# Performance work log

Hardware: AMD Instinct MI355X
Metric: run time of the kernel (lower is better)

Reference implementation:

```python
import jax, jax.numpy as jnp
import numpy as np

N = 10000       # nodes (atoms)
E = 160000      # edges (avg degree 16)
NE = 10         # num_elements
C = 64          # hidden scalar channels (hidden_irreps 0e multiplicity)
NB = 8          # num_bessel
SH = 9          # spherical-harmonic dim for max_ell=2 (1+3+5)
MLPH = 16       # readout MLP hidden (MLP_irreps)
T = 2           # num_interactions
R_MAX = 5.0
P_CUT = 6       # num_polynomial_cutoff
AVG_NEIGH = 32.0


def _sph(u):
    # real spherical harmonics up to l=2, e3nn 'component' normalization
    x, y, z = u[:, 0], u[:, 1], u[:, 2]
    s3, s5, s15 = 3.0 ** 0.5, 5.0 ** 0.5, 15.0 ** 0.5
    return jnp.stack([
        jnp.ones_like(x),
        s3 * x, s3 * y, s3 * z,
        s15 * x * y, s15 * y * z, (s5 / 2) * (3 * z * z - 1),
        s15 * x * z, (s15 / 2) * (x * x - y * y)], axis=-1)


def _radial(r):
    # Bessel radial basis * smooth polynomial cutoff (RadialEmbeddingBlock)
    n = jnp.arange(1, NB + 1, dtype=r.dtype)
    bessel = (2.0 / R_MAX) ** 0.5 * jnp.sin(n * jnp.pi * r[:, None] / R_MAX) / r[:, None]
    x = jnp.clip(r / R_MAX, 0.0, 1.0)
    p = P_CUT
    fc = (1.0 - 0.5 * (p + 1) * (p + 2) * x ** p
          + p * (p + 2) * x ** (p + 1)
          - 0.5 * p * (p + 1) * x ** (p + 2))
    fc = jnp.where(x < 1.0, fc, 0.0)
    return bessel * fc[:, None]


def setup_inputs():
    key = jax.random.key(0)
    ks = jax.random.split(key, 14)
    positions = jax.random.normal(ks[0], (N, 3), jnp.float32) * 3.0
    node_attrs = jax.nn.one_hot(jax.random.randint(ks[1], (N,), 0, NE), NE, dtype=jnp.float32)
    edge_index = jax.random.randint(ks[2], (2, E), 0, N)
    shifts = jnp.zeros((E, 3), jnp.float32)

    def g(k, shape, fan):
        return jax.random.normal(k, shape, jnp.float32) / np.sqrt(fan)

    params = dict(
        atomic_energies=jax.random.normal(ks[3], (NE,), jnp.float32),
        W_embed=g(ks[4], (NE, C), NE),          # LinearNodeEmbeddingBlock
        W_up=g(ks[5], (T, C, C), C),            # linear_up per interaction
        W_r1=g(ks[6], (T, NB, MLPH), NB),       # radial MLP layer 1
        W_r2=g(ks[7], (T, MLPH, C * SH), MLPH), # radial MLP -> TP weights
        W_mix=g(ks[8], (T, C, SH, C), C * SH),  # post-scatter linear mixing
        W_self=g(ks[9], (T, C, C), C),          # self/skip connection
        w_read=g(ks[10], (C,), C),              # LinearReadoutBlock
        W_mlp1=g(ks[11], (C, MLPH), C),         # NonLinearReadoutBlock
        w_mlp2=g(ks[12], (MLPH,), MLPH),
    )
    return dict(positions=positions, node_attrs=node_attrs, shifts=shifts,
                edge_index=edge_index, **params)


def reference(positions, node_attrs, shifts, atomic_energies, W_embed, W_up,
              W_r1, W_r2, W_mix, W_self, w_read, W_mlp1, w_mlp2, edge_index):
    snd, rcv = edge_index[0], edge_index[1]
    vec = positions[rcv] - positions[snd] + shifts              # [E,3]
    r = jnp.linalg.norm(vec, axis=-1) + 1e-9                    # [E]
    sh = _sph(vec / r[:, None])                                 # [E,SH]
    edge_feats = _radial(r)                                     # [E,NB]

    h = node_attrs @ W_embed                                    # [N,C] node embedding
    reps = [node_attrs @ atomic_energies]                       # node_e0
    for t in range(T):
        h_up = h @ W_up[t]                                      # [N,C]
        # radial-MLP produced tensor-product weights, one per (channel, sh) path
        tp_w = (jax.nn.silu(edge_feats @ W_r1[t]) @ W_r2[t]).reshape(-1, C, SH)
        # gather -> edge-wise tensor product -> scatter-reduce (the hot loop)
        msg = tp_w * h_up[snd][:, :, None] * sh[:, None, :]     # [E,C,SH]
        agg = jax.ops.segment_sum(msg, rcv, num_segments=N) / AVG_NEIGH
        h = jnp.einsum('ncs,cso->no', agg, W_mix[t]) + h @ W_self[t]
        if t < T - 1:
            reps.append(h @ w_read)                             # linear readout
        else:
            reps.append(jax.nn.silu(h @ W_mlp1) @ w_mlp2)       # nonlinear readout
    return jnp.stack(reps, axis=0)  # [T+1, N] per-layer atomic energy contributions
```

## Files before the change

### kernel.cpp

```cpp
#include <hip/hip_runtime.h>
#include <math.h>

#define N_NODES 10000
#define N_EDGES 160000
#define NEL 10
#define C 64
#define NB 8
#define SHD 9
#define MLPH 16
#define CSH 576
#define R_MAX 5.0f
#define INV_AVG 0.03125f
#define SCAN_CH 40
#define WBASE (N_EDGES - 2 * 8 * CSH)
#define WB2   (WBASE - 10240)
#define WB3   (WB2 - 1024)
#define ROWP  584

typedef _Float16 f16x2 __attribute__((ext_vector_type(2)));
typedef _Float16 f16x8 __attribute__((ext_vector_type(8)));
typedef float    f32x4 __attribute__((ext_vector_type(4)));
typedef _Float16 half_t;

__device__ __forceinline__ float silu_f(float v) {
    return v / (1.0f + __expf(-v));
}

__device__ __forceinline__ float dot2f(f16x2 a, f16x2 b, float c) {
#if __has_builtin(__builtin_amdgcn_fdot2)
    return __builtin_amdgcn_fdot2(a, b, c, false);
#else
    return c + (float)a.x * (float)b.x + (float)a.y * (float)b.y;
#endif
}

__global__ __launch_bounds__(256) void k_zero(
    int* __restrict__ cnt, int* __restrict__ deg)
{
    int i = blockIdx.x * 256 + threadIdx.x;
    if (i == 0) *cnt = 0;
    if (i < N_NODES) deg[i] = 0;
}

__global__ __launch_bounds__(256) void k_edge(
    const float* __restrict__ pos, const float* __restrict__ shifts,
    const int* __restrict__ ei,
    const float* __restrict__ na, const float* __restrict__ We,
    const float* __restrict__ ae,
    int* __restrict__ cnt, int* __restrict__ deg,
    int* __restrict__ act_snd, int* __restrict__ act_rcv,
    float* __restrict__ act_u, float* __restrict__ act_ef,
    half_t* __restrict__ hh, float* __restrict__ out)
{
    int i = blockIdx.x * 256 + threadIdx.x;
    int lane = threadIdx.x & 63;

    {
        int n = i >> 6;
        float acc = 0.0f, e0 = 0.0f;
        #pragma unroll
        for (int k = 0; k < NEL; k++) {
            float a = na[n * NEL + k];
            acc += a * We[k * C + lane];
            e0 += a * ae[k];
        }
        hh[i] = (half_t)acc;
        if (lane == 0) out[n] = e0;
    }

    if (blockIdx.x >= N_EDGES / 256) return;
    int e = i;
    int snd = ei[e];
    int rcv = ei[N_EDGES + e];
    float vx = pos[rcv * 3 + 0] - pos[snd * 3 + 0] + shifts[e * 3 + 0];
    float vy = pos[rcv * 3 + 1] - pos[snd * 3 + 1] + shifts[e * 3 + 1];
    float vz = pos[rcv * 3 + 2] - pos[snd * 3 + 2] + shifts[e * 3 + 2];
    float r = sqrtf(vx * vx + vy * vy + vz * vz) + 1e-9f;
    float x = r / R_MAX;
    bool active = x < 1.0f;

    unsigned long long m = __ballot(active);
    int base = 0;
    if (m) {
        int leader = __ffsll((unsigned long long)m) - 1;
        if (lane == leader) base = atomicAdd(cnt, __popcll(m));
        base = __shfl(base, leader);
    }
    if (!active) return;

    int p = base + __popcll(m & ((1ull << lane) - 1ull));
    act_snd[p] = snd;
    act_rcv[p] = rcv;
    atomicAdd(&deg[rcv], 1);

    float inv_r = 1.0f / r;
    *(float4*)&act_u[p * 4] = make_float4(vx * inv_r, vy * inv_r, vz * inv_r, r);

    float x6 = x * x * x; x6 = x6 * x6;
    float x7 = x6 * x;
    float x8 = x7 * x;
    float fc = 1.0f - 28.0f * x6 + 48.0f * x7 - 21.0f * x8;
    float theta = 3.14159265358979323846f * r / R_MAX;
    float s1 = sinf(theta), c1 = cosf(theta);
    float sn = s1, cn = c1;
    float scale = 0.6324555320336759f * inv_r * fc;
    float ef[NB];
    ef[0] = scale * sn;
    #pragma unroll
    for (int n = 1; n < NB; n++) {
        float sn1 = sn * c1 + cn * s1;
        float cn1 = cn * c1 - sn * s1;
        sn = sn1; cn = cn1;
        ef[n] = scale * sn;
    }
    *(float4*)&act_ef[p * 8 + 0] = make_float4(ef[0], ef[1], ef[2], ef[3]);
    *(float4*)&act_ef[p * 8 + 4] = make_float4(ef[4], ef[5], ef[6], ef[7]);
}

__global__ __launch_bounds__(256) void k_scan(
    const int* __restrict__ deg, int* __restrict__ rowptr, int* __restrict__ cursor)
{
    __shared__ int dl[N_NODES];
    __shared__ int part[256];
    int tid = threadIdx.x;
    for (int i = tid; i < N_NODES; i += 256) dl[i] = deg[i];
    __syncthreads();

    int base = tid * SCAN_CH;
    int s = 0;
    #pragma unroll 8
    for (int i = 0; i < SCAN_CH; i++) {
        int idx = base + i;
        if (idx < N_NODES) s += dl[idx];
    }
    part[tid] = s;
    __syncthreads();
    for (int off = 1; off < 256; off <<= 1) {
        int v = (tid >= off) ? part[tid - off] : 0;
        __syncthreads();
        part[tid] += v;
        __syncthreads();
    }
    int run = part[tid] - s;
    for (int i = 0; i < SCAN_CH; i++) {
        int idx = base + i;
        if (idx < N_NODES) {
            int v = dl[idx];
            dl[idx] = run;
            run += v;
        }
    }
    __syncthreads();
    for (int i = tid; i < N_NODES; i += 256) {
        int r = dl[i];
        rowptr[i] = r;
        cursor[i] = r;
    }
    if (tid == 255) rowptr[N_NODES] = part[255];
}

__global__ __launch_bounds__(256) void k_rank(
    const int* __restrict__ cnt, const int* __restrict__ act_rcv,
    const float* __restrict__ Wr2, const float* __restrict__ Wmix,
    const float* __restrict__ Wself, const float* __restrict__ Wup,
    int* __restrict__ cursor, f16x2* __restrict__ wlth,
    f16x8* __restrict__ wmixf, f16x8* __restrict__ wupf, int* __restrict__ perm)
{
    int i = blockIdx.x * 256 + threadIdx.x;
    int nAct = *cnt;

    if (i >= WBASE) {
        int idx = i - WBASE;
        int t = idx / (8 * CSH);
        int r = idx - t * (8 * CSH);
        int mq = r / CSH, j = r - mq * CSH;
        int c = j & 63, s = j >> 6;
        float lo = Wr2[t * MLPH * CSH + (2 * mq + 0) * CSH + c * SHD + s];
        float hi = Wr2[t * MLPH * CSH + (2 * mq + 1) * CSH + c * SHD + s];
        f16x2 v; v.x = (_Float16)lo; v.y = (_Float16)hi;
        wlth[idx] = v;
    } else if (i >= WB2) {
        int idx = i - WB2;
        int t = idx / 5120;
        int r = idx - t * 5120;
        int ks = r >> 8;
        int rr = r & 255;
        int nt = rr >> 6;
        int ln = rr & 63;
        f16x8 v;
        #pragma unroll
        for (int e = 0; e < 8; e++) {
            int k = ks * 32 + ((ln >> 4) << 3) + e;
            int col = nt * 16 + (ln & 15);
            float x;
            if (k < CSH)
                x = Wmix[(size_t)t * CSH * C + ((k & 63) * SHD + (k >> 6)) * C + col] * INV_AVG;
            else
                x = Wself[(size_t)t * C * C + (k - CSH) * C + col];
            v[e] = (_Float16)x;
        }
        wmixf[(size_t)((t * 20 + ks) * 4 + nt) * 64 + ln] = v;
    } else if (i >= WB3) {
        int idx = i - WB3;
        int t = idx >> 9;
        int r = idx & 511;
        int ks = r >> 8;
        int rr = r & 255;
        int nt = rr >> 6;
        int ln = rr & 63;
        f16x8 v;
        #pragma unroll
        for (int e = 0; e < 8; e++) {
            int k = ks * 32 + ((ln >> 4) << 3) + e;
            int col = nt * 16 + (ln & 15);
            v[e] = (_Float16)Wup[(size_t)t * C * C + k * C + col];
        }
        wupf[(size_t)((t * 2 + ks) * 4 + nt) * 64 + ln] = v;
    }
    if (i >= nAct) return;
    int pos = atomicAdd(&cursor[act_rcv[i]], 1);
    perm[pos] = i;
}

__global__ __launch_bounds__(256) void k_permute(
    const int* __restrict__ cnt, const int* __restrict__ perm,
    const int* __restrict__ act_snd, const int* __restrict__ act_rcv,
    const float* __restrict__ act_u, const float* __restrict__ act_ef,
    const float* __restrict__ Wr1,
    int* __restrict__ csnd, int* __restrict__ crcv, float* __restrict__ csh,
    f16x2* __restrict__ chidh0, f16x2* __restrict__ chidh1)
{
    int p = blockIdx.x * 256 + threadIdx.x;
    if (p >= *cnt) return;
    int i = perm[p];

    csnd[p] = act_snd[i];
    crcv[p] = act_rcv[i];

    float4 u4 = *(const float4*)&act_u[i * 4];
    float ux = u4.x, uy = u4.y, uz = u4.z;
    const float s3 = 1.7320508075688772f;
    const float s5 = 2.23606797749979f;
    const float s15 = 3.872983346207417f;
    *(float4*)&csh[p * 16 + 0] = make_float4(1.0f, s3 * ux, s3 * uy, s3 * uz);
    *(float4*)&csh[p * 16 + 4] = make_float4(s15 * ux * uy, s15 * uy * uz,
                                             0.5f * s5 * (3.0f * uz * uz - 1.0f),
                                             s15 * ux * uz);
    csh[p * 16 + 8] = 0.5f * s15 * (ux * ux - uy * uy);

    float4 e0 = *(const float4*)&act_ef[i * 8 + 0];
    float4 e1 = *(const float4*)&act_ef[i * 8 + 4];
    float ef[NB] = {e0.x, e0.y, e0.z, e0.w, e1.x, e1.y, e1.z, e1.w};

    #pragma unroll
    for (int t = 0; t < 2; t++) {
        f16x2* dst = (t == 0) ? chidh0 : chidh1;
        const float* W = Wr1 + t * NB * MLPH;
        f16x2 hv2[8];
        #pragma unroll
        for (int mp = 0; mp < 8; mp++) {
            float a0 = 0.0f, a1 = 0.0f;
            #pragma unroll
            for (int b = 0; b < NB; b++) {
                float efb = ef[b];
                a0 += efb * W[b * MLPH + 2 * mp + 0];
                a1 += efb * W[b * MLPH + 2 * mp + 1];
            }
            f16x2 v; v.x = (_Float16)silu_f(a0); v.y = (_Float16)silu_f(a1);
            hv2[mp] = v;
        }
        *(float4*)&dst[p * 8 + 0] = *(float4*)&hv2[0];
        *(float4*)&dst[p * 8 + 4] = *(float4*)&hv2[4];
    }
}

__global__ __launch_bounds__(64) void k_upm(
    const half_t* __restrict__ hh, const f16x8* __restrict__ wupf,
    float* __restrict__ hup)
{
    int lane = threadIdx.x & 63;
    int base = blockIdx.x * 16;
    int rowA = base + (lane & 15);
    int kg = (lane >> 4) << 3;

    f32x4 u0 = {0.f,0.f,0.f,0.f}, u1 = {0.f,0.f,0.f,0.f};
    f32x4 u2 = {0.f,0.f,0.f,0.f}, u3 = {0.f,0.f,0.f,0.f};
    const half_t* hrow = hh + (size_t)rowA * C + kg;
    #pragma unroll
    for (int ks = 0; ks < 2; ks++) {
        f16x8 a = *(const f16x8*)(hrow + ks * 32);
        const f16x8* bp = wupf + (size_t)(ks * 4) * 64 + lane;
        u0 = __builtin_amdgcn_mfma_f32_16x16x32_f16(a, bp[0],   u0, 0, 0, 0);
        u1 = __builtin_amdgcn_mfma_f32_16x16x32_f16(a, bp[64],  u1, 0, 0, 0);
        u2 = __builtin_amdgcn_mfma_f32_16x16x32_f16(a, bp[128], u2, 0, 0, 0);
        u3 = __builtin_amdgcn_mfma_f32_16x16x32_f16(a, bp[192], u3, 0, 0, 0);
    }
    int colb = lane & 15;
    int rowb = base + ((lane >> 4) << 2);
    #pragma unroll
    for (int r = 0; r < 4; r++) {
        float* hp = hup + (size_t)(rowb + r) * C + colb;
        hp[0]  = u0[r];
        hp[16] = u1[r];
        hp[32] = u2[r];
        hp[48] = u3[r];
    }
}

template <int RMODE>
__global__ __launch_bounds__(256) void k_fuse(
    const int* __restrict__ rowptr, const int* __restrict__ csnd,
    const int* __restrict__ crcv, const float* __restrict__ csh,
    const f16x2* __restrict__ chh, const f16x2* __restrict__ wlth,
    const float* __restrict__ hup_in, const f16x8* __restrict__ wf,
    const f16x8* __restrict__ wupf1, half_t* __restrict__ hh,
    const float* __restrict__ wread, const float* __restrict__ Wm1,
    const float* __restrict__ wm2,
    float* __restrict__ hup_out, float* __restrict__ rep)
{
    __shared__ half_t Hs[16 * ROWP];
    __shared__ half_t Hs2[16 * 72];

    int lane = threadIdx.x & 63;
    int w = threadIdx.x >> 6;
    int bbase = blockIdx.x * 16;
    int n0 = bbase + w * 4;
    int beg = rowptr[n0], end = rowptr[n0 + 4];

    f16x2 wreg[8][9];
    #pragma unroll
    for (int mq = 0; mq < 8; mq++)
        #pragma unroll
        for (int jj = 0; jj < 9; jj++)
            wreg[mq][jj] = wlth[mq * CSH + (jj << 6) + lane];

    float acc[9];
    int curRcv = -1;

#define FLUSH() { half_t* ag = &Hs[(curRcv - bbase) * ROWP + lane]; \
    _Pragma("unroll") for (int jj = 0; jj < 9; jj++) ag[jj << 6] = (half_t)acc[jj]; }
#define ZFILL(FROM, TO) for (int zn = (FROM); zn < (TO); zn++) { \
    half_t* ag = &Hs[(zn - bbase) * ROWP + lane]; \
    _Pragma("unroll") for (int jj = 0; jj < 9; jj++) ag[jj << 6] = (half_t)0.0f; }

    for (int k0 = beg; k0 < end; k0 += 4) {
        int nv = end - k0; if (nv > 4) nv = 4;

#define PRE(Q) int kc##Q = (k0 + Q < end) ? k0 + Q : end - 1; \
        int rcvq##Q = crcv[kc##Q]; \
        float hupq##Q = hup_in[csnd[kc##Q] * C + lane];
        PRE(0) PRE(1) PRE(2) PRE(3)
#undef PRE

        float tw0[9], tw1[9], tw2[9], tw3[9];
        #pragma unroll
        for (int jj = 0; jj < 9; jj++) {
            tw0[jj] = 0.f; tw1[jj] = 0.f; tw2[jj] = 0.f; tw3[jj] = 0.f;
        }

        #pragma unroll
        for (int mq = 0; mq < 8; mq++) {
            f16x2 h0 = chh[kc0 * 8 + mq], h1 = chh[kc1 * 8 + mq];
            f16x2 h2 = chh[kc2 * 8 + mq], h3 = chh[kc3 * 8 + mq];
            #pragma unroll
            for (int jj = 0; jj < 9; jj++) {
                f16x2 wv = wreg[mq][jj];
                tw0[jj] = dot2f(h0, wv, tw0[jj]);
                tw1[jj] = dot2f(h1, wv, tw1[jj]);
                tw2[jj] = dot2f(h2, wv, tw2[jj]);
                tw3[jj] = dot2f(h3, wv, tw3[jj]);
            }
        }

#define SCAT(Q) if (Q < nv) { \
        int rcv = rcvq##Q; \
        float hupS = hupq##Q; \
        float4 sA = *(const float4*)&csh[kc##Q * 16]; \
        float4 sB = *(const float4*)&csh[kc##Q * 16 + 4]; \
        float s8v = csh[kc##Q * 16 + 8]; \
        float sh9[9] = {sA.x, sA.y, sA.z, sA.w, sB.x, sB.y, sB.z, sB.w, s8v}; \
        if (rcv != curRcv) { \
            if (curRcv >= 0) { FLUSH(); ZFILL(curRcv + 1, rcv) } else { ZFILL(n0, rcv) } \
            curRcv = rcv; \
            _Pragma("unroll") for (int jj = 0; jj < 9; jj++) acc[jj] = tw##Q[jj] * (hupS * sh9[jj]); \
        } else { \
            _Pragma("unroll") for (int jj = 0; jj < 9; jj++) acc[jj] += tw##Q[jj] * (hupS * sh9[jj]); \
        } }
        SCAT(0) SCAT(1) SCAT(2) SCAT(3)
#undef SCAT
    }

    int zfrom = n0;
    if (curRcv >= 0) { FLUSH(); zfrom = curRcv + 1; }
    ZFILL(zfrom, n0 + 4)
#undef FLUSH
#undef ZFILL

    __syncthreads();

    int rowL = lane & 15;
    int kg = (lane >> 4) << 3;
    f32x4 acc4 = {0.f, 0.f, 0.f, 0.f};
    const half_t* hrow = hh + (size_t)(bbase + rowL) * C + kg;
    #pragma unroll
    for (int ks = 0; ks < 20; ks++) {
        f16x8 a = (ks < 18) ? *(const f16x8*)&Hs[rowL * ROWP + ks * 32 + kg]
                            : *(const f16x8*)(hrow + (ks - 18) * 32);
        f16x8 b = wf[(size_t)(ks * 4 + w) * 64 + lane];
        acc4 = __builtin_amdgcn_mfma_f32_16x16x32_f16(a, b, acc4, 0, 0, 0);
    }

    int colb = lane & 15;
    int rq = (lane >> 4) << 2;

    __syncthreads();

    if (RMODE == 0) {
        #pragma unroll
        for (int r = 0; r < 4; r++)
            Hs2[(rq + r) * 72 + w * 16 + colb] = (half_t)acc4[r];
        __syncthreads();

        if (w == 0) {
            int row = lane & 15, seg = lane >> 4;
            float v = 0.0f;
            #pragma unroll
            for (int j = 0; j < 16; j++)
                v += (float)Hs2[row * 72 + seg * 16 + j] * wread[seg * 16 + j];
            v += __shfl_xor(v, 16);
            v += __shfl_xor(v, 32);
            if (seg == 0) rep[bbase + row] = v;
        }

        {
            int idx = threadIdx.x;
            if (idx < 128) {
                int row = idx >> 3, cq = idx & 7;
                *(float4*)&hh[(size_t)(bbase + row) * C + cq * 8] =
                    *(const float4*)&Hs2[row * 72 + cq * 8];
            }
        }

        f32x4 u = {0.f, 0.f, 0.f, 0.f};
        #pragma unroll
        for (int ks = 0; ks < 2; ks++) {
            f16x8 a = *(const f16x8*)&Hs2[rowL * 72 + ks * 32 + kg];
            f16x8 b = wupf1[(size_t)(ks * 4 + w) * 64 + lane];
            u = __builtin_amdgcn_mfma_f32_16x16x32_f16(a, b, u, 0, 0, 0);
        }
        #pragma unroll
        for (int r = 0; r < 4; r++)
            hup_out[(size_t)(bbase + rq + r) * C + w * 16 + colb] = u[r];
    } else {
        float* Hn = (float*)Hs;
        float* W1l = (float*)Hs + 16 * 68;
        for (int t = threadIdx.x; t < C * MLPH; t += 256) W1l[t] = Wm1[t];
        #pragma unroll
        for (int r = 0; r < 4; r++)
            Hn[(rq + r) * 68 + w * 16 + colb] = acc4[r];
        __syncthreads();

        int n = threadIdx.x >> 4, m = threadIdx.x & 15;
        float a2 = 0.0f;
        #pragma unroll 8
        for (int c = 0; c < C; c++) a2 += Hn[n * 68 + c] * W1l[c * MLPH + m];
        float rv = silu_f(a2) * wm2[m];
        rv += __shfl_xor(rv, 1); rv += __shfl_xor(rv, 2);
        rv += __shfl_xor(rv, 4); rv += __shfl_xor(rv, 8);
        if (m == 0) rep[bbase + n] = rv;
    }
}

extern "C" void kernel_launch(void* const* d_in, const int* in_sizes, int n_in,
                              void* d_out, int out_size, void* d_ws, size_t ws_size,
                              hipStream_t stream) {
    const float* pos    = (const float*)d_in[0];
    const float* na     = (const float*)d_in[1];
    const float* shifts = (const float*)d_in[2];
    const int*   ei     = (const int*)d_in[3];
    const float* ae     = (const float*)d_in[4];
    const float* We     = (const float*)d_in[5];
    const float* Wup    = (const float*)d_in[6];
    const float* Wr1    = (const float*)d_in[7];
    const float* Wr2    = (const float*)d_in[8];
    const float* Wmix   = (const float*)d_in[9];
    const float* Wself  = (const float*)d_in[10];
    const float* wread  = (const float*)d_in[11];
    const float* Wm1    = (const float*)d_in[12];
    const float* wm2    = (const float*)d_in[13];
    float* out = (float*)d_out;

    char* ws = (char*)d_ws;
    size_t off = 0;
    auto alloc = [&](size_t bytes) {
        off = (off + 255) & ~(size_t)255;
        void* p = ws + off;
        off += bytes;
        return p;
    };
    int*   cnt     = (int*)alloc(4);
    int*   deg     = (int*)alloc((size_t)N_NODES * 4);
    int*   rowptr  = (int*)alloc((size_t)(N_NODES + 1) * 4);
    int*   cursor  = (int*)alloc((size_t)N_NODES * 4);
    f16x2* wlth    = (f16x2*)alloc((size_t)2 * 8 * CSH * 4);
    f16x8* wmixf   = (f16x8*)alloc((size_t)2 * 5120 * 16);
    f16x8* wupf    = (f16x8*)alloc((size_t)1024 * 16);
    int*   perm    = (int*)alloc((size_t)N_EDGES * 4);
    int*   act_snd = (int*)alloc((size_t)N_EDGES * 4);
    int*   act_rcv = (int*)alloc((size_t)N_EDGES * 4);
    float* act_u   = (float*)alloc((size_t)N_EDGES * 4 * 4);
    float* act_ef  = (float*)alloc((size_t)N_EDGES * 8 * 4);
    int*   csnd    = (int*)alloc((size_t)N_EDGES * 4);
    int*   crcv    = (int*)alloc((size_t)N_EDGES * 4);
    float* csh     = (float*)alloc((size_t)N_EDGES * 16 * 4);
    f16x2* chidh0  = (f16x2*)alloc((size_t)N_EDGES * 8 * 4);
    f16x2* chidh1  = (f16x2*)alloc((size_t)N_EDGES * 8 * 4);
    float* hup     = (float*)alloc((size_t)N_NODES * C * 4);
    float* hup2    = (float*)alloc((size_t)N_NODES * C * 4);
    half_t* hh     = (half_t*)alloc((size_t)N_NODES * C * 2);

    k_zero<<<(N_NODES + 255) / 256, 256, 0, stream>>>(cnt, deg);

    k_edge<<<(N_NODES * C) / 256, 256, 0, stream>>>(pos, shifts, ei, na, We, ae,
                                                    cnt, deg, act_snd, act_rcv,
                                                    act_u, act_ef, hh, out);
    k_scan<<<1, 256, 0, stream>>>(deg, rowptr, cursor);
    k_rank<<<N_EDGES / 256, 256, 0, stream>>>(cnt, act_rcv, Wr2, Wmix, Wself, Wup,
                                              cursor, wlth, wmixf, wupf, perm);
    k_permute<<<N_EDGES / 256, 256, 0, stream>>>(cnt, perm, act_snd, act_rcv,
                                                 act_u, act_ef, Wr1,
                                                 csnd, crcv, csh, chidh0, chidh1);
    k_upm<<<N_NODES / 16, 64, 0, stream>>>(hh, wupf, hup);

    k_fuse<0><<<N_NODES / 16, 256, 0, stream>>>(rowptr, csnd, crcv, csh,
                                                chidh0, wlth, hup,
                                                wmixf, wupf + 512, hh,
                                                wread, Wm1, wm2,
                                                hup2, out + N_NODES);

    k_fuse<1><<<N_NODES / 16, 256, 0, stream>>>(rowptr, csnd, crcv, csh,
                                                chidh1, wlth + 8 * CSH, hup2,
                                                wmixf + 5120, wupf + 512, hh,
                                                wread, Wm1, wm2,
                                                hup, out + 2 * N_NODES);
}
```

Before: 123.4 us.

## Merge rank and permute into one atomic scatter, halve nodes per fuse block

Weight repacking moves into the spare blocks of k_edge. The separate k_rank and k_permute kernels are replaced by a single k_scatter that claims its CSR slot with an atomicAdd and writes the permuted edge data directly, removing the perm array and one launch. k_fuse now handles 8 nodes per block instead of 16, doubling the grid to improve load balance and occupancy. The cost is that the 16-row MFMA tiles are half wasted, and edge order within a node's segment is now nondeterministic.

```diff
diff --git a/kernel.cpp b/kernel.cpp
--- a/kernel.cpp
+++ b/kernel.cpp
@@ -12,10 +12,8 @@
 #define R_MAX 5.0f
 #define INV_AVG 0.03125f
 #define SCAN_CH 40
-#define WBASE (N_EDGES - 2 * 8 * CSH)
-#define WB2   (WBASE - 10240)
-#define WB3   (WB2 - 1024)
 #define ROWP  584
+#define NPB   8
 
 typedef _Float16 f16x2 __attribute__((ext_vector_type(2)));
 typedef _Float16 f16x8 __attribute__((ext_vector_type(8)));
@@ -47,9 +45,12 @@
     const int* __restrict__ ei,
     const float* __restrict__ na, const float* __restrict__ We,
     const float* __restrict__ ae,
+    const float* __restrict__ Wr2, const float* __restrict__ Wmix,
+    const float* __restrict__ Wself, const float* __restrict__ Wup,
     int* __restrict__ cnt, int* __restrict__ deg,
     int* __restrict__ act_snd, int* __restrict__ act_rcv,
     float* __restrict__ act_u, float* __restrict__ act_ef,
+    f16x2* __restrict__ wlth, f16x8* __restrict__ wmixf, f16x8* __restrict__ wupf,
     half_t* __restrict__ hh, float* __restrict__ out)
 {
     int i = blockIdx.x * 256 + threadIdx.x;
@@ -68,7 +69,58 @@
         if (lane == 0) out[n] = e0;
     }
 
-    if (blockIdx.x >= N_EDGES / 256) return;
+    if (blockIdx.x >= N_EDGES / 256) {
+        int idx = i - N_EDGES;
+        if (idx < 2 * 8 * CSH) {
+            int t = idx / (8 * CSH);
+            int r = idx - t * (8 * CSH);
+            int mq = r / CSH, j = r - mq * CSH;
+            int c = j & 63, s = j >> 6;
+            float lo = Wr2[t * MLPH * CSH + (2 * mq + 0) * CSH + c * SHD + s];
+            float hi = Wr2[t * MLPH * CSH + (2 * mq + 1) * CSH + c * SHD + s];
+            f16x2 v; v.x = (_Float16)lo; v.y = (_Float16)hi;
+            wlth[idx] = v;
+        } else if (idx < 2 * 8 * CSH + 10240) {
+            int k2 = idx - 2 * 8 * CSH;
+            int t = k2 / 5120;
+            int r = k2 - t * 5120;
+            int ks = r >> 8;
+            int rr = r & 255;
+            int nt = rr >> 6;
+            int ln = rr & 63;
+            f16x8 v;
+            #pragma unroll
+            for (int e = 0; e < 8; e++) {
+                int k = ks * 32 + ((ln >> 4) << 3) + e;
+                int col = nt * 16 + (ln & 15);
+                float x;
+                if (k < CSH)
+                    x = Wmix[(size_t)t * CSH * C + ((k & 63) * SHD + (k >> 6)) * C + col] * INV_AVG;
+                else
+                    x = Wself[(size_t)t * C * C + (k - CSH) * C + col];
+                v[e] = (_Float16)x;
+            }
+            wmixf[(size_t)((t * 20 + ks) * 4 + nt) * 64 + ln] = v;
+        } else if (idx < 2 * 8 * CSH + 10240 + 1024) {
+            int k2 = idx - (2 * 8 * CSH + 10240);
+            int t = k2 >> 9;
+            int r = k2 & 511;
+            int ks = r >> 8;
+            int rr = r & 255;
+            int nt = rr >> 6;
+            int ln = rr & 63;
+            f16x8 v;
+            #pragma unroll
+            for (int e = 0; e < 8; e++) {
+                int k = ks * 32 + ((ln >> 4) << 3) + e;
+                int col = nt * 16 + (ln & 15);
+                v[e] = (_Float16)Wup[(size_t)t * C * C + k * C + col];
+            }
+            wupf[(size_t)((t * 2 + ks) * 4 + nt) * 64 + ln] = v;
+        }
+        return;
+    }
+
     int e = i;
     int snd = ei[e];
     int rcv = ei[N_EDGES + e];
@@ -159,83 +211,21 @@
     if (tid == 255) rowptr[N_NODES] = part[255];
 }
 
-__global__ __launch_bounds__(256) void k_rank(
-    const int* __restrict__ cnt, const int* __restrict__ act_rcv,
-    const float* __restrict__ Wr2, const float* __restrict__ Wmix,
-    const float* __restrict__ Wself, const float* __restrict__ Wup,
-    int* __restrict__ cursor, f16x2* __restrict__ wlth,
-    f16x8* __restrict__ wmixf, f16x8* __restrict__ wupf, int* __restrict__ perm)
-{
-    int i = blockIdx.x * 256 + threadIdx.x;
-    int nAct = *cnt;
-
-    if (i >= WBASE) {
-        int idx = i - WBASE;
-        int t = idx / (8 * CSH);
-        int r = idx - t * (8 * CSH);
-        int mq = r / CSH, j = r - mq * CSH;
-        int c = j & 63, s = j >> 6;
-        float lo = Wr2[t * MLPH * CSH + (2 * mq + 0) * CSH + c * SHD + s];
-        float hi = Wr2[t * MLPH * CSH + (2 * mq + 1) * CSH + c * SHD + s];
-        f16x2 v; v.x = (_Float16)lo; v.y = (_Float16)hi;
-        wlth[idx] = v;
-    } else if (i >= WB2) {
-        int idx = i - WB2;
-        int t = idx / 5120;
-        int r = idx - t * 5120;
-        int ks = r >> 8;
-        int rr = r & 255;
-        int nt = rr >> 6;
-        int ln = rr & 63;
-        f16x8 v;
-        #pragma unroll
-        for (int e = 0; e < 8; e++) {
-            int k = ks * 32 + ((ln >> 4) << 3) + e;
-            int col = nt * 16 + (ln & 15);
-            float x;
-            if (k < CSH)
-                x = Wmix[(size_t)t * CSH * C + ((k & 63) * SHD + (k >> 6)) * C + col] * INV_AVG;
-            else
-                x = Wself[(size_t)t * C * C + (k - CSH) * C + col];
-            v[e] = (_Float16)x;
-        }
-        wmixf[(size_t)((t * 20 + ks) * 4 + nt) * 64 + ln] = v;
-    } else if (i >= WB3) {
-        int idx = i - WB3;
-        int t = idx >> 9;
-        int r = idx & 511;
-        int ks = r >> 8;
-        int rr = r & 255;
-        int nt = rr >> 6;
-        int ln = rr & 63;
-        f16x8 v;
-        #pragma unroll
-        for (int e = 0; e < 8; e++) {
-            int k = ks * 32 + ((ln >> 4) << 3) + e;
-            int col = nt * 16 + (ln & 15);
-            v[e] = (_Float16)Wup[(size_t)t * C * C + k * C + col];
-        }
-        wupf[(size_t)((t * 2 + ks) * 4 + nt) * 64 + ln] = v;
-    }
-    if (i >= nAct) return;
-    int pos = atomicAdd(&cursor[act_rcv[i]], 1);
-    perm[pos] = i;
-}
-
-__global__ __launch_bounds__(256) void k_permute(
-    const int* __restrict__ cnt, const int* __restrict__ perm,
-    const int* __restrict__ act_snd, const int* __restrict__ act_rcv,
-    const float* __restrict__ act_u, const float* __restrict__ act_ef,
-    const float* __restrict__ Wr1,
+__global__ __launch_bounds__(256) void k_scatter(
+    const int* __restrict__ cnt, const int* __restrict__ act_snd,
+    const int* __restrict__ act_rcv, const float* __restrict__ act_u,
+    const float* __restrict__ act_ef, const float* __restrict__ Wr1,
+    int* __restrict__ cursor,
     int* __restrict__ csnd, int* __restrict__ crcv, float* __restrict__ csh,
     f16x2* __restrict__ chidh0, f16x2* __restrict__ chidh1)
 {
-    int p = blockIdx.x * 256 + threadIdx.x;
-    if (p >= *cnt) return;
-    int i = perm[p];
+    int i = blockIdx.x * 256 + threadIdx.x;
+    if (i >= *cnt) return;
+    int rcv = act_rcv[i];
+    int p = atomicAdd(&cursor[rcv], 1);
 
     csnd[p] = act_snd[i];
-    crcv[p] = act_rcv[i];
+    crcv[p] = rcv;
 
     float4 u4 = *(const float4*)&act_u[i * 4];
     float ux = u4.x, uy = u4.y, uz = u4.z;
@@ -318,14 +308,16 @@
     const float* __restrict__ wm2,
     float* __restrict__ hup_out, float* __restrict__ rep)
 {
-    __shared__ half_t Hs[16 * ROWP];
-    __shared__ half_t Hs2[16 * 72];
+    __shared__ half_t Hs[NPB * ROWP];
+    __shared__ half_t Hs2[NPB * 72];
+    __shared__ float  Hn[NPB * 68];
+    __shared__ float  W1l[C * MLPH];
 
     int lane = threadIdx.x & 63;
     int w = threadIdx.x >> 6;
-    int bbase = blockIdx.x * 16;
-    int n0 = bbase + w * 4;
-    int beg = rowptr[n0], end = rowptr[n0 + 4];
+    int bbase = blockIdx.x * NPB;
+    int n0 = bbase + w * 2;
+    int beg = rowptr[n0], end = rowptr[n0 + 2];
 
     f16x2 wreg[8][9];
     #pragma unroll
@@ -392,19 +384,20 @@
 
     int zfrom = n0;
     if (curRcv >= 0) { FLUSH(); zfrom = curRcv + 1; }
-    ZFILL(zfrom, n0 + 4)
+    ZFILL(zfrom, n0 + 2)
 #undef FLUSH
 #undef ZFILL
 
     __syncthreads();
 
     int rowL = lane & 15;
+    int rowS = rowL & 7;
     int kg = (lane >> 4) << 3;
     f32x4 acc4 = {0.f, 0.f, 0.f, 0.f};
-    const half_t* hrow = hh + (size_t)(bbase + rowL) * C + kg;
+    const half_t* hrow = hh + (size_t)(bbase + rowS) * C + kg;
     #pragma unroll
     for (int ks = 0; ks < 20; ks++) {
-        f16x8 a = (ks < 18) ? *(const f16x8*)&Hs[rowL * ROWP + ks * 32 + kg]
+        f16x8 a = (ks < 18) ? *(const f16x8*)&Hs[rowS * ROWP + ks * 32 + kg]
                             : *(const f16x8*)(hrow + (ks - 18) * 32);
         f16x8 b = wf[(size_t)(ks * 4 + w) * 64 + lane];
         acc4 = __builtin_amdgcn_mfma_f32_16x16x32_f16(a, b, acc4, 0, 0, 0);
@@ -412,29 +405,34 @@
 
     int colb = lane & 15;
     int rq = (lane >> 4) << 2;
+    bool storeR = rq < NPB;
 
     __syncthreads();
 
     if (RMODE == 0) {
-        #pragma unroll
-        for (int r = 0; r < 4; r++)
-            Hs2[(rq + r) * 72 + w * 16 + colb] = (half_t)acc4[r];
+        if (storeR) {
+            #pragma unroll
+            for (int r = 0; r < 4; r++)
+                Hs2[(rq + r) * 72 + w * 16 + colb] = (half_t)acc4[r];
+        }
         __syncthreads();
 
         if (w == 0) {
             int row = lane & 15, seg = lane >> 4;
             float v = 0.0f;
-            #pragma unroll
-            for (int j = 0; j < 16; j++)
-                v += (float)Hs2[row * 72 + seg * 16 + j] * wread[seg * 16 + j];
+            if (row < NPB) {
+                #pragma unroll
+                for (int j = 0; j < 16; j++)
+                    v += (float)Hs2[row * 72 + seg * 16 + j] * wread[seg * 16 + j];
+            }
             v += __shfl_xor(v, 16);
             v += __shfl_xor(v, 32);
-            if (seg == 0) rep[bbase + row] = v;
+            if (seg == 0 && row < NPB) rep[bbase + row] = v;
         }
 
         {
             int idx = threadIdx.x;
-            if (idx < 128) {
+            if (idx < 64) {
                 int row = idx >> 3, cq = idx & 7;
                 *(float4*)&hh[(size_t)(bbase + row) * C + cq * 8] =
                     *(const float4*)&Hs2[row * 72 + cq * 8];
@@ -444,30 +442,34 @@
         f32x4 u = {0.f, 0.f, 0.f, 0.f};
         #pragma unroll
         for (int ks = 0; ks < 2; ks++) {
-            f16x8 a = *(const f16x8*)&Hs2[rowL * 72 + ks * 32 + kg];
+            f16x8 a = *(const f16x8*)&Hs2[rowS * 72 + ks * 32 + kg];
             f16x8 b = wupf1[(size_t)(ks * 4 + w) * 64 + lane];
             u = __builtin_amdgcn_mfma_f32_16x16x32_f16(a, b, u, 0, 0, 0);
         }
-        #pragma unroll
-        for (int r = 0; r < 4; r++)
-            hup_out[(size_t)(bbase + rq + r) * C + w * 16 + colb] = u[r];
+        if (storeR) {
+            #pragma unroll
+            for (int r = 0; r < 4; r++)
+                hup_out[(size_t)(bbase + rq + r) * C + w * 16 + colb] = u[r];
+        }
     } else {
-        float* Hn = (float*)Hs;
-        float* W1l = (float*)Hs + 16 * 68;
         for (int t = threadIdx.x; t < C * MLPH; t += 256) W1l[t] = Wm1[t];
-        #pragma unroll
-        for (int r = 0; r < 4; r++)
-            Hn[(rq + r) * 68 + w * 16 + colb] = acc4[r];
+        if (storeR) {
+            #pragma unroll
+            for (int r = 0; r < 4; r++)
+                Hn[(rq + r) * 68 + w * 16 + colb] = acc4[r];
+        }
         __syncthreads();
 
         int n = threadIdx.x >> 4, m = threadIdx.x & 15;
-        float a2 = 0.0f;
-        #pragma unroll 8
-        for (int c = 0; c < C; c++) a2 += Hn[n * 68 + c] * W1l[c * MLPH + m];
-        float rv = silu_f(a2) * wm2[m];
-        rv += __shfl_xor(rv, 1); rv += __shfl_xor(rv, 2);
-        rv += __shfl_xor(rv, 4); rv += __shfl_xor(rv, 8);
-        if (m == 0) rep[bbase + n] = rv;
+        if (n < NPB) {
+            float a2 = 0.0f;
+            #pragma unroll 8
+            for (int c = 0; c < C; c++) a2 += Hn[n * 68 + c] * W1l[c * MLPH + m];
+            float rv = silu_f(a2) * wm2[m];
+            rv += __shfl_xor(rv, 1); rv += __shfl_xor(rv, 2);
+            rv += __shfl_xor(rv, 4); rv += __shfl_xor(rv, 8);
+            if (m == 0) rep[bbase + n] = rv;
+        }
     }
 }
 
@@ -505,7 +507,6 @@
     f16x2* wlth    = (f16x2*)alloc((size_t)2 * 8 * CSH * 4);
     f16x8* wmixf   = (f16x8*)alloc((size_t)2 * 5120 * 16);
     f16x8* wupf    = (f16x8*)alloc((size_t)1024 * 16);
-    int*   perm    = (int*)alloc((size_t)N_EDGES * 4);
     int*   act_snd = (int*)alloc((size_t)N_EDGES * 4);
     int*   act_rcv = (int*)alloc((size_t)N_EDGES * 4);
     float* act_u   = (float*)alloc((size_t)N_EDGES * 4 * 4);
@@ -522,25 +523,25 @@
     k_zero<<<(N_NODES + 255) / 256, 256, 0, stream>>>(cnt, deg);
 
     k_edge<<<(N_NODES * C) / 256, 256, 0, stream>>>(pos, shifts, ei, na, We, ae,
+                                                    Wr2, Wmix, Wself, Wup,
                                                     cnt, deg, act_snd, act_rcv,
-                                                    act_u, act_ef, hh, out);
+                                                    act_u, act_ef,
+                                                    wlth, wmixf, wupf, hh, out);
+    k_upm<<<N_NODES / 16, 64, 0, stream>>>(hh, wupf, hup);
     k_scan<<<1, 256, 0, stream>>>(deg, rowptr, cursor);
-    k_rank<<<N_EDGES / 256, 256, 0, stream>>>(cnt, act_rcv, Wr2, Wmix, Wself, Wup,
-                                              cursor, wlth, wmixf, wupf, perm);
-    k_permute<<<N_EDGES / 256, 256, 0, stream>>>(cnt, perm, act_snd, act_rcv,
-                                                 act_u, act_ef, Wr1,
+    k_scatter<<<N_EDGES / 256, 256, 0, stream>>>(cnt, act_snd, act_rcv,
+                                                 act_u, act_ef, Wr1, cursor,
                                                  csnd, crcv, csh, chidh0, chidh1);
-    k_upm<<<N_NODES / 16, 64, 0, stream>>>(hh, wupf, hup);
-
-    k_fuse<0><<<N_NODES / 16, 256, 0, stream>>>(rowptr, csnd, crcv, csh,
-                                                chidh0, wlth, hup,
-                                                wmixf, wupf + 512, hh,
-                                                wread, Wm1, wm2,
-                                                hup2, out + N_NODES);
-
-    k_fuse<1><<<N_NODES / 16, 256, 0, stream>>>(rowptr, csnd, crcv, csh,
-                                                chidh1, wlth + 8 * CSH, hup2,
-                                                wmixf + 5120, wupf + 512, hh,
-                                                wread, Wm1, wm2,
-                                                hup, out + 2 * N_NODES);
-}
+
+    k_fuse<0><<<N_NODES / NPB, 256, 0, stream>>>(rowptr, csnd, crcv, csh,
+                                                 chidh0, wlth, hup,
+                                                 wmixf, wupf + 512, hh,
+                                                 wread, Wm1, wm2,
+                                                 hup2, out + N_NODES);
+
+    k_fuse<1><<<N_NODES / NPB, 256, 0, stream>>>(rowptr, csnd, crcv, csh,
+                                                 chidh1, wlth + 8 * CSH, hup2,
+                                                 wmixf + 5120, wupf + 512, hh,
+                                                 wread, Wm1, wm2,
+                                                 hup, out + 2 * N_NODES);
+}
```

New measurement: 124.6 us. Within noise of the previous version (+1.0%).
